# Kernel optimization log

Hardware: AMD Instinct MI355X
Metric: run time of the kernel (lower is better)

Reference implementation:

```python
import jax, jax.numpy as jnp
import numpy as np

B, N, XS, YS, KS, D, V = 32, 32, 256, 256, 128, 1024, 32000
TAU = 1e-4

def setup_inputs() -> dict:
    key = jax.random.key(0)
    ks = jax.random.split(key, 12)
    return {
        'utterence_hidden': jax.random.normal(ks[0], (XS, B, D), jnp.float32),
        'response_hidden': jax.random.normal(ks[1], (YS, B, D), jnp.float32),
        'knowledge_hidden': jax.random.normal(ks[2], (N, KS, B, D), jnp.float32),
        'utterence_pad_mask': jax.random.bernoulli(ks[3], 0.1, (B, XS)),
        'response_pad_mask': jax.random.bernoulli(ks[4], 0.1, (B, YS)),
        'knowledge_pad_mask': jax.random.bernoulli(ks[5], 0.1, (B, N, KS)),
        'gumbel': jax.random.gumbel(ks[6], (B, N), jnp.float32),
        'W1': jax.random.normal(ks[7], (D, 2 * D), jnp.float32) * 0.02,
        'b1': jnp.zeros((D,), jnp.float32),
        'W2': jax.random.normal(ks[8], (V, D), jnp.float32) * 0.02,
        'b2': jnp.zeros((V,), jnp.float32),
    }

def reference(utterence_hidden, response_hidden, knowledge_hidden,
              utterence_pad_mask, response_pad_mask, knowledge_pad_mask,
              gumbel, W1, b1, W2, b2):
    # make_pad_embed_zero's eye-matrix bmm/einsum is mathematically just masking
    uh = jnp.transpose(utterence_hidden, (1, 0, 2)) * (~utterence_pad_mask)[:, :, None]   # (B,XS,D)
    rh = jnp.transpose(response_hidden, (1, 0, 2)) * (~response_pad_mask)[:, :, None]     # (B,YS,D)
    kh = jnp.transpose(knowledge_hidden, (2, 0, 1, 3)) * (~knowledge_pad_mask)[..., None] # (B,N,KS,D)
    # AvgPool2d over full seq length == sum / seq_len (zeros included)
    mean_X = jnp.sum(uh, axis=1) / XS          # (B,D)
    mean_Y = jnp.sum(rh, axis=1) / YS          # (B,D)
    mean_K = jnp.sum(kh, axis=2) / KS          # (B,N,D)
    prior = jax.nn.log_softmax(jnp.einsum('bd,bnd->bn', mean_X, mean_K), axis=1)  # (B,N)
    X_cat_Y = jnp.concatenate([mean_X, mean_Y], axis=1) @ W1.T + b1               # (B,D)
    posterior_logits = jnp.einsum('bd,bnd->bn', X_cat_Y, mean_K)                  # (B,N)
    posterior = jax.nn.softmax(posterior_logits, axis=1)
    # gumbel_softmax with tau=1e-4 (soft, near one-hot)
    K_index = jax.nn.softmax((posterior_logits + gumbel) / TAU, axis=1)           # (B,N)
    selected_K = jnp.einsum('bnsd,bn->bsd', kh, K_index)                          # (B,KS,D)
    vocab_selected_K = jnp.einsum('bnd,bn->bd', mean_K, K_index)                  # (B,D)
    vocab_selected_K = jax.nn.log_softmax(vocab_selected_K @ W2.T + b2, axis=1)   # (B,V)
    return (prior, posterior, K_index, selected_K, vocab_selected_K)
```

## Files before the change

### kernel.cpp

```cpp
#include <hip/hip_runtime.h>
#include <math.h>

#define BB 32
#define NN 32
#define XSS 256
#define KSS 128
#define DD 1024
#define VV 32000
#define TAU_INV 10000.0f

typedef int mask_t;

#define WS_MEANX   0
#define WS_MEANY   32768
#define WS_MEANK   65536
#define WS_XCATY   1114112
#define WS_VPRE    1146880
#define WS_NNZ_CNT 1179648
#define WS_NNZ_IDX 1179680
#define WS_NNZ_W   1180704
#define WS_LSM_M   1181728
#define WS_LSM_S   1182240
#define WS_LSE     1182752

#define OUT_PRIOR  0
#define OUT_POST   (BB*NN)
#define OUT_KIDX   (2*BB*NN)
#define OUT_SEL    (3*BB*NN)
#define OUT_VOCAB  (3*BB*NN + BB*KSS*DD)

__device__ __forceinline__ float dot4(float4 a, float4 b) {
  return a.x*b.x + a.y*b.y + a.z*b.z + a.w*b.w;
}

__global__ void k_meanxy(const float4* __restrict__ U, const float4* __restrict__ R,
                         const mask_t* __restrict__ um, const mask_t* __restrict__ rm,
                         float* __restrict__ ws) {
  const int chunk = blockIdx.x, b = blockIdx.y, which = blockIdx.z, t = threadIdx.x;
  const float4* src = which ? R : U;
  const mask_t* m = which ? rm : um;
  float* dst = ws + (which ? WS_MEANY : WS_MEANX) + b * DD;
  float4 acc = make_float4(0.f, 0.f, 0.f, 0.f);
  const int x0 = chunk * 32;
  for (int x = x0; x < x0 + 32; ++x) {
    if (!m[b * XSS + x]) {
      float4 v = src[(x * BB + b) * (DD/4) + t];
      acc.x += v.x; acc.y += v.y; acc.z += v.z; acc.w += v.w;
    }
  }
  const float s = 1.0f / XSS;
  atomicAdd(&dst[t*4+0], acc.x * s);
  atomicAdd(&dst[t*4+1], acc.y * s);
  atomicAdd(&dst[t*4+2], acc.z * s);
  atomicAdd(&dst[t*4+3], acc.w * s);
}

__global__ void k_meank(const float4* __restrict__ K, const mask_t* __restrict__ km,
                        float* __restrict__ ws) {
  const int n = blockIdx.x, b = blockIdx.y, t = threadIdx.x;
  const mask_t* mrow = km + (b * NN + n) * KSS;
  float4 acc = make_float4(0.f, 0.f, 0.f, 0.f);
  #pragma unroll 2
  for (int s = 0; s < KSS; ++s) {
    if (!mrow[s]) {
      float4 v = K[((n * KSS + s) * BB + b) * (DD/4) + t];
      acc.x += v.x; acc.y += v.y; acc.z += v.z; acc.w += v.w;
    }
  }
  const float sc = 1.0f / KSS;
  float4* out = (float4*)(ws + WS_MEANK) + (b * NN + n) * (DD/4);
  out[t] = make_float4(acc.x*sc, acc.y*sc, acc.z*sc, acc.w*sc);
}

__global__ void k_xcaty(const float4* __restrict__ W1, const float* __restrict__ b1,
                        float* __restrict__ ws) {
  const int t = threadIdx.x;
  const int b = t & 31;
  const int d = blockIdx.x * 8 + (t >> 5);
  const float4* mx = (const float4*)(ws + WS_MEANX) + b * (DD/4);
  const float4* my = (const float4*)(ws + WS_MEANY) + b * (DD/4);
  const float4* w  = W1 + d * (2 * DD / 4);
  float acc = b1[d];
  #pragma unroll 4
  for (int q = 0; q < DD/4; ++q) acc += dot4(w[q], mx[q]);
  #pragma unroll 4
  for (int q = 0; q < DD/4; ++q) acc += dot4(w[DD/4 + q], my[q]);
  ws[WS_XCATY + b * DD + d] = acc;
}

__global__ void k_small(const float* __restrict__ gumbel, float* __restrict__ ws,
                        float* __restrict__ out) {
  const int b = blockIdx.x, t = threadIdx.x;
  const int lane = t & 63, wid = t >> 6;
  __shared__ float redp[4], redq[4];
  __shared__ float plp[NN], plq[NN], kw[NN];
  __shared__ float scal[3];
  __shared__ int   nnz_idx_s[NN];
  __shared__ float nnz_w_s[NN];
  __shared__ int   nnz_cnt_s;

  const float4* mk = (const float4*)(ws + WS_MEANK) + b * NN * (DD/4);
  const float4 mxr = ((const float4*)(ws + WS_MEANX))[b * (DD/4) + t];
  const float4 xyr = ((const float4*)(ws + WS_XCATY))[b * (DD/4) + t];

  for (int n = 0; n < NN; ++n) {
    float4 mkv = mk[n * (DD/4) + t];
    float pp = dot4(mkv, mxr);
    float qq = dot4(mkv, xyr);
    for (int off = 32; off > 0; off >>= 1) {
      pp += __shfl_down(pp, off);
      qq += __shfl_down(qq, off);
    }
    if (lane == 0) { redp[wid] = pp; redq[wid] = qq; }
    __syncthreads();
    if (t == 0) {
      plp[n] = redp[0] + redp[1] + redp[2] + redp[3];
      plq[n] = redq[0] + redq[1] + redq[2] + redq[3];
    }
    __syncthreads();
  }

  if (t == 0) {
    float z[NN];
    float m1 = -1e30f, m2 = -1e30f, m3 = -1e30f;
    for (int n = 0; n < NN; ++n) {
      m1 = fmaxf(m1, plp[n]);
      m2 = fmaxf(m2, plq[n]);
      z[n] = plq[n] + gumbel[b * NN + n];
      m3 = fmaxf(m3, z[n]);
    }
    float s1 = 0.f, s2 = 0.f, s3 = 0.f;
    for (int n = 0; n < NN; ++n) {
      s1 += expf(plp[n] - m1);
      s2 += expf(plq[n] - m2);
      float w = expf((z[n] - m3) * TAU_INV);
      kw[n] = w;
      s3 += w;
    }
    scal[0] = m1 + logf(s1);
    scal[1] = m2;
    scal[2] = s2;
    const float inv3 = 1.0f / s3;
    int cnt = 0;
    for (int n = 0; n < NN; ++n) {
      kw[n] *= inv3;
      if (kw[n] > 0.f) { nnz_idx_s[cnt] = n; nnz_w_s[cnt] = kw[n]; ++cnt; }
    }
    nnz_cnt_s = cnt;
    ((int*)(ws + WS_NNZ_CNT))[b] = cnt;
    for (int j = 0; j < cnt; ++j) {
      ((int*)(ws + WS_NNZ_IDX))[b * NN + j] = nnz_idx_s[j];
      ws[WS_NNZ_W + b * NN + j] = nnz_w_s[j];
    }
  }
  __syncthreads();

  if (t < NN) {
    out[OUT_PRIOR + b * NN + t] = plp[t] - scal[0];
    out[OUT_POST  + b * NN + t] = expf(plq[t] - scal[1]) / scal[2];
    out[OUT_KIDX  + b * NN + t] = kw[t];
  }

  float4 acc = make_float4(0.f, 0.f, 0.f, 0.f);
  const int cnt = nnz_cnt_s;
  for (int j = 0; j < cnt; ++j) {
    const float w = nnz_w_s[j];
    float4 v = mk[nnz_idx_s[j] * (DD/4) + t];
    acc.x += w * v.x; acc.y += w * v.y; acc.z += w * v.z; acc.w += w * v.w;
  }
  ((float4*)(ws + WS_VPRE))[b * (DD/4) + t] = acc;
}

__global__ void k_selected(const float4* __restrict__ K, const mask_t* __restrict__ km,
                           const float* __restrict__ ws, float4* __restrict__ outsel) {
  const int s = blockIdx.x, b = blockIdx.y, t = threadIdx.x;
  const int cnt = ((const int*)(ws + WS_NNZ_CNT))[b];
  float4 acc = make_float4(0.f, 0.f, 0.f, 0.f);
  for (int j = 0; j < cnt; ++j) {
    const int n = ((const int*)(ws + WS_NNZ_IDX))[b * NN + j];
    const float w = ws[WS_NNZ_W + b * NN + j];
    if (!km[(b * NN + n) * KSS + s]) {
      float4 v = K[((n * KSS + s) * BB + b) * (DD/4) + t];
      acc.x += w * v.x; acc.y += w * v.y; acc.z += w * v.z; acc.w += w * v.w;
    }
  }
  outsel[(b * KSS + s) * (DD/4) + t] = acc;
}

__global__ void __launch_bounds__(256) k_vocab(const float4* __restrict__ W2,
                                               const float* __restrict__ ws,
                                               float* __restrict__ logits) {
  const int t = threadIdx.x;
  const int V0 = blockIdx.x * 256;
  const int e4_base = blockIdx.y * 128;
  __shared__ float4 w2s[256 * 9];
  __shared__ float4 pres[32 * 9];
  const float4* vp = (const float4*)(ws + WS_VPRE);
  const int vlane = t & 31, bgrp = t >> 5;

  float acc[8][4];
  #pragma unroll
  for (int k = 0; k < 8; ++k)
    #pragma unroll
    for (int j = 0; j < 4; ++j) acc[k][j] = 0.f;

  for (int e4 = e4_base; e4 < e4_base + 128; e4 += 8) {
    #pragma unroll
    for (int k = 0; k < 8; ++k) {
      const int f = t + 256 * k;
      const int vr = f >> 3, q = f & 7;
      w2s[vr * 9 + q] = W2[(V0 + vr) * (DD/4) + e4 + q];
    }
    {
      const int br = t >> 3, q = t & 7;
      pres[br * 9 + q] = vp[br * (DD/4) + e4 + q];
    }
    __syncthreads();
    #pragma unroll
    for (int q = 0; q < 8; ++q) {
      float4 pb[4];
      #pragma unroll
      for (int j = 0; j < 4; ++j) pb[j] = pres[(bgrp + 8 * j) * 9 + q];
      #pragma unroll
      for (int k = 0; k < 8; ++k) {
        float4 wv = w2s[(vlane + 32 * k) * 9 + q];
        #pragma unroll
        for (int j = 0; j < 4; ++j) acc[k][j] += dot4(wv, pb[j]);
      }
    }
    __syncthreads();
  }
  #pragma unroll
  for (int k = 0; k < 8; ++k)
    #pragma unroll
    for (int j = 0; j < 4; ++j)
      atomicAdd(&logits[(bgrp + 8 * j) * VV + V0 + vlane + 32 * k], acc[k][j]);
}

__global__ void k_lsm1(const float* __restrict__ logits, const float* __restrict__ b2,
                       float* __restrict__ ws) {
  const int c = blockIdx.x, b = blockIdx.y, t = threadIdx.x;
  const int lane = t & 63, wid = t >> 6;
  const float* base = logits + b * VV + c * 2000;
  const float* bb = b2 + c * 2000;
  __shared__ float red[4];
  float xv[8];
  int cnt = 0;
  float m = -1e30f;
  for (int i = t; i < 2000; i += 256) {
    float x = base[i] + bb[i];
    xv[cnt++] = x;
    m = fmaxf(m, x);
  }
  for (int off = 32; off > 0; off >>= 1) m = fmaxf(m, __shfl_down(m, off));
  if (lane == 0) red[wid] = m;
  __syncthreads();
  if (t == 0) red[0] = fmaxf(fmaxf(red[0], red[1]), fmaxf(red[2], red[3]));
  __syncthreads();
  const float M = red[0];
  __syncthreads();
  float s = 0.f;
  for (int i = 0; i < cnt; ++i) s += expf(xv[i] - M);
  for (int off = 32; off > 0; off >>= 1) s += __shfl_down(s, off);
  if (lane == 0) red[wid] = s;
  __syncthreads();
  if (t == 0) {
    ws[WS_LSM_M + b * 16 + c] = M;
    ws[WS_LSM_S + b * 16 + c] = red[0] + red[1] + red[2] + red[3];
  }
}

__global__ void k_lsm2(float* __restrict__ ws) {
  const int t = threadIdx.x;
  if (t < BB) {
    float M = -1e30f;
    for (int c = 0; c < 16; ++c) M = fmaxf(M, ws[WS_LSM_M + t * 16 + c]);
    float S = 0.f;
    for (int c = 0; c < 16; ++c)
      S += ws[WS_LSM_S + t * 16 + c] * expf(ws[WS_LSM_M + t * 16 + c] - M);
    ws[WS_LSE + t] = M + logf(S);
  }
}

__global__ void k_lsm3(const float* __restrict__ b2, const float* __restrict__ ws,
                       float* __restrict__ logits) {
  const int v = blockIdx.x * 256 + threadIdx.x;
  const int b = blockIdx.y;
  logits[b * VV + v] = logits[b * VV + v] + b2[v] - ws[WS_LSE + b];
}

extern "C" void kernel_launch(void* const* d_in, const int* in_sizes, int n_in,
                              void* d_out, int out_size, void* d_ws, size_t ws_size,
                              hipStream_t stream) {
  const float4* U  = (const float4*)d_in[0];
  const float4* R  = (const float4*)d_in[1];
  const float4* K  = (const float4*)d_in[2];
  const mask_t* um = (const mask_t*)d_in[3];
  const mask_t* rm = (const mask_t*)d_in[4];
  const mask_t* km = (const mask_t*)d_in[5];
  const float* g   = (const float*)d_in[6];
  const float4* W1 = (const float4*)d_in[7];
  const float* b1  = (const float*)d_in[8];
  const float4* W2 = (const float4*)d_in[9];
  const float* b2  = (const float*)d_in[10];
  float* out = (float*)d_out;
  float* ws  = (float*)d_ws;

  hipMemsetAsync(ws + WS_MEANX, 0, 2 * BB * DD * sizeof(float), stream);
  hipMemsetAsync(out + OUT_VOCAB, 0, (size_t)BB * VV * sizeof(float), stream);

  k_meanxy <<<dim3(8, 32, 2), 256, 0, stream>>>(U, R, um, rm, ws);
  k_meank  <<<dim3(NN, BB),   256, 0, stream>>>(K, km, ws);
  k_xcaty  <<<dim3(128),      256, 0, stream>>>(W1, b1, ws);
  k_small  <<<dim3(BB),       256, 0, stream>>>(g, ws, out);
  k_selected<<<dim3(KSS, BB), 256, 0, stream>>>(K, km, ws, (float4*)(out + OUT_SEL));
  k_vocab  <<<dim3(125, 2),   256, 0, stream>>>(W2, ws, out + OUT_VOCAB);
  k_lsm1   <<<dim3(16, BB),   256, 0, stream>>>(out + OUT_VOCAB, b2, ws);
  k_lsm2   <<<dim3(1),        64,  0, stream>>>(ws);
  k_lsm3   <<<dim3(125, BB),  256, 0, stream>>>(b2, ws, out + OUT_VOCAB);
}
```

Measured before the change: 986.4 us.

## Rework mean, xcaty, small and vocab kernels; drop atomics and a launch

Several kernels change at once. k_meanxy uses a branchless mask-weighted loop over larger chunks. k_meank compacts unmasked rows with a ballot so that four loads are in flight at a time. k_xcaty tiles W1 and the inputs through shared memory so each weight is reused across batches. k_small reduces per wave with no per-n barriers, and k_vocab writes two partial buffers instead of doing atomicAdd, which removes the memset and the k_lsm2 launch. This adds workspace traffic for the partial logits, but the work is mostly bound by the memory read of K.

```diff
diff --git a/kernel.cpp b/kernel.cpp
--- a/kernel.cpp
+++ b/kernel.cpp
@@ -21,7 +21,8 @@
 #define WS_NNZ_W   1180704
 #define WS_LSM_M   1181728
 #define WS_LSM_S   1182240
-#define WS_LSE     1182752
+#define WS_VP0     1183744
+#define WS_VP1     2207744
 
 #define OUT_PRIOR  0
 #define OUT_POST   (BB*NN)
@@ -31,6 +32,9 @@
 
 __device__ __forceinline__ float dot4(float4 a, float4 b) {
   return a.x*b.x + a.y*b.y + a.z*b.z + a.w*b.w;
+}
+__device__ __forceinline__ void fma4(float4& a, float w, float4 v) {
+  a.x += w*v.x; a.y += w*v.y; a.z += w*v.z; a.w += w*v.w;
 }
 
 __global__ void k_meanxy(const float4* __restrict__ U, const float4* __restrict__ R,
@@ -40,13 +44,15 @@
   const float4* src = which ? R : U;
   const mask_t* m = which ? rm : um;
   float* dst = ws + (which ? WS_MEANY : WS_MEANX) + b * DD;
+  __shared__ float wmask[64];
+  const int x0 = chunk * 64;
+  if (t < 64) wmask[t] = m[b * XSS + x0 + t] ? 0.f : 1.f;
+  __syncthreads();
   float4 acc = make_float4(0.f, 0.f, 0.f, 0.f);
-  const int x0 = chunk * 32;
-  for (int x = x0; x < x0 + 32; ++x) {
-    if (!m[b * XSS + x]) {
-      float4 v = src[(x * BB + b) * (DD/4) + t];
-      acc.x += v.x; acc.y += v.y; acc.z += v.z; acc.w += v.w;
-    }
+  #pragma unroll 4
+  for (int i = 0; i < 64; ++i) {
+    float4 v = src[((x0 + i) * BB + b) * (DD/4) + t];
+    fma4(acc, wmask[i], v);
   }
   const float s = 1.0f / XSS;
   atomicAdd(&dst[t*4+0], acc.x * s);
@@ -58,41 +64,90 @@
 __global__ void k_meank(const float4* __restrict__ K, const mask_t* __restrict__ km,
                         float* __restrict__ ws) {
   const int n = blockIdx.x, b = blockIdx.y, t = threadIdx.x;
+  const int lane = t & 63, wid = t >> 6;
+  __shared__ int idx[KSS];
+  __shared__ int wcnt[2];
   const mask_t* mrow = km + (b * NN + n) * KSS;
-  float4 acc = make_float4(0.f, 0.f, 0.f, 0.f);
-  #pragma unroll 2
-  for (int s = 0; s < KSS; ++s) {
-    if (!mrow[s]) {
-      float4 v = K[((n * KSS + s) * BB + b) * (DD/4) + t];
-      acc.x += v.x; acc.y += v.y; acc.z += v.z; acc.w += v.w;
-    }
+  bool keep = false; int pre = 0;
+  if (t < KSS) {
+    keep = !mrow[t];
+    unsigned long long mb = __ballot(keep);
+    pre = __popcll(mb & ((1ull << lane) - 1ull));
+    if (lane == 0) wcnt[wid] = __popcll(mb);
+  }
+  __syncthreads();
+  if (t < KSS && keep) {
+    const int base = wid ? wcnt[0] : 0;
+    idx[base + pre] = t;
+  }
+  __syncthreads();
+  const int cnt = wcnt[0] + wcnt[1];
+  const float4* Kb = K + (size_t)b * (DD/4);
+  const size_t srow = (size_t)BB * (DD/4);
+  float4 a = make_float4(0.f, 0.f, 0.f, 0.f);
+  int j = 0;
+  for (; j + 4 <= cnt; j += 4) {
+    const int s0 = idx[j], s1 = idx[j+1], s2 = idx[j+2], s3 = idx[j+3];
+    float4 v0 = Kb[(size_t)(n*KSS + s0) * srow + t];
+    float4 v1 = Kb[(size_t)(n*KSS + s1) * srow + t];
+    float4 v2 = Kb[(size_t)(n*KSS + s2) * srow + t];
+    float4 v3 = Kb[(size_t)(n*KSS + s3) * srow + t];
+    a.x += (v0.x + v1.x) + (v2.x + v3.x);
+    a.y += (v0.y + v1.y) + (v2.y + v3.y);
+    a.z += (v0.z + v1.z) + (v2.z + v3.z);
+    a.w += (v0.w + v1.w) + (v2.w + v3.w);
+  }
+  for (; j < cnt; ++j) {
+    float4 v = Kb[(size_t)(n*KSS + idx[j]) * srow + t];
+    a.x += v.x; a.y += v.y; a.z += v.z; a.w += v.w;
   }
   const float sc = 1.0f / KSS;
-  float4* out = (float4*)(ws + WS_MEANK) + (b * NN + n) * (DD/4);
-  out[t] = make_float4(acc.x*sc, acc.y*sc, acc.z*sc, acc.w*sc);
+  ((float4*)(ws + WS_MEANK))[(b * NN + n) * (DD/4) + t] =
+      make_float4(a.x*sc, a.y*sc, a.z*sc, a.w*sc);
 }
 
 __global__ void k_xcaty(const float4* __restrict__ W1, const float* __restrict__ b1,
                         float* __restrict__ ws) {
+  __shared__ float4 xys[32][33];
+  __shared__ float4 w1s[16][33];
   const int t = threadIdx.x;
-  const int b = t & 31;
-  const int d = blockIdx.x * 8 + (t >> 5);
-  const float4* mx = (const float4*)(ws + WS_MEANX) + b * (DD/4);
-  const float4* my = (const float4*)(ws + WS_MEANY) + b * (DD/4);
-  const float4* w  = W1 + d * (2 * DD / 4);
-  float acc = b1[d];
-  #pragma unroll 4
-  for (int q = 0; q < DD/4; ++q) acc += dot4(w[q], mx[q]);
-  #pragma unroll 4
-  for (int q = 0; q < DD/4; ++q) acc += dot4(w[DD/4 + q], my[q]);
-  ws[WS_XCATY + b * DD + d] = acc;
+  const int d0 = blockIdx.x * 16;
+  const int dl = t >> 4, bg = t & 15;
+  const float4* mx = (const float4*)(ws + WS_MEANX);
+  const float4* my = (const float4*)(ws + WS_MEANY);
+  float acc[2] = {0.f, 0.f};
+  for (int c = 0; c < 16; ++c) {
+    #pragma unroll
+    for (int i = 0; i < 4; ++i) {
+      const int f = t + 256 * i;
+      const int br = f >> 5, q = f & 31;
+      const int kf4 = c * 32 + q;
+      xys[br][q] = (kf4 < 256) ? mx[br * 256 + kf4] : my[br * 256 + (kf4 - 256)];
+    }
+    #pragma unroll
+    for (int i = 0; i < 2; ++i) {
+      const int f = t + 256 * i;
+      const int dr = f >> 5, q = f & 31;
+      w1s[dr][q] = W1[(d0 + dr) * (2*DD/4) + c * 32 + q];
+    }
+    __syncthreads();
+    #pragma unroll
+    for (int q = 0; q < 32; ++q) {
+      const float4 wv = w1s[dl][q];
+      acc[0] += dot4(wv, xys[bg*2+0][q]);
+      acc[1] += dot4(wv, xys[bg*2+1][q]);
+    }
+    __syncthreads();
+  }
+  const float bias = b1[d0 + dl];
+  ws[WS_XCATY + (bg*2+0) * DD + d0 + dl] = acc[0] + bias;
+  ws[WS_XCATY + (bg*2+1) * DD + d0 + dl] = acc[1] + bias;
 }
 
 __global__ void k_small(const float* __restrict__ gumbel, float* __restrict__ ws,
                         float* __restrict__ out) {
   const int b = blockIdx.x, t = threadIdx.x;
   const int lane = t & 63, wid = t >> 6;
-  __shared__ float redp[4], redq[4];
   __shared__ float plp[NN], plq[NN], kw[NN];
   __shared__ float scal[3];
   __shared__ int   nnz_idx_s[NN];
@@ -100,25 +155,25 @@
   __shared__ int   nnz_cnt_s;
 
   const float4* mk = (const float4*)(ws + WS_MEANK) + b * NN * (DD/4);
-  const float4 mxr = ((const float4*)(ws + WS_MEANX))[b * (DD/4) + t];
-  const float4 xyr = ((const float4*)(ws + WS_XCATY))[b * (DD/4) + t];
-
-  for (int n = 0; n < NN; ++n) {
-    float4 mkv = mk[n * (DD/4) + t];
-    float pp = dot4(mkv, mxr);
-    float qq = dot4(mkv, xyr);
+  const float4* mx = (const float4*)(ws + WS_MEANX) + b * (DD/4);
+  const float4* xy = (const float4*)(ws + WS_XCATY) + b * (DD/4);
+
+  for (int n = wid; n < NN; n += 4) {
+    float pp = 0.f, qq = 0.f;
+    #pragma unroll
+    for (int r = 0; r < 4; ++r) {
+      const int q = r * 64 + lane;
+      const float4 mkv = mk[n * (DD/4) + q];
+      pp += dot4(mkv, mx[q]);
+      qq += dot4(mkv, xy[q]);
+    }
     for (int off = 32; off > 0; off >>= 1) {
       pp += __shfl_down(pp, off);
       qq += __shfl_down(qq, off);
     }
-    if (lane == 0) { redp[wid] = pp; redq[wid] = qq; }
-    __syncthreads();
-    if (t == 0) {
-      plp[n] = redp[0] + redp[1] + redp[2] + redp[3];
-      plq[n] = redq[0] + redq[1] + redq[2] + redq[3];
-    }
-    __syncthreads();
-  }
+    if (lane == 0) { plp[n] = pp; plq[n] = qq; }
+  }
+  __syncthreads();
 
   if (t == 0) {
     float z[NN];
@@ -165,8 +220,7 @@
   const int cnt = nnz_cnt_s;
   for (int j = 0; j < cnt; ++j) {
     const float w = nnz_w_s[j];
-    float4 v = mk[nnz_idx_s[j] * (DD/4) + t];
-    acc.x += w * v.x; acc.y += w * v.y; acc.z += w * v.z; acc.w += w * v.w;
+    fma4(acc, w, mk[nnz_idx_s[j] * (DD/4) + t]);
   }
   ((float4*)(ws + WS_VPRE))[b * (DD/4) + t] = acc;
 }
@@ -180,19 +234,18 @@
     const int n = ((const int*)(ws + WS_NNZ_IDX))[b * NN + j];
     const float w = ws[WS_NNZ_W + b * NN + j];
     if (!km[(b * NN + n) * KSS + s]) {
-      float4 v = K[((n * KSS + s) * BB + b) * (DD/4) + t];
-      acc.x += w * v.x; acc.y += w * v.y; acc.z += w * v.z; acc.w += w * v.w;
+      fma4(acc, w, K[((n * KSS + s) * BB + b) * (DD/4) + t]);
     }
   }
   outsel[(b * KSS + s) * (DD/4) + t] = acc;
 }
 
 __global__ void __launch_bounds__(256) k_vocab(const float4* __restrict__ W2,
-                                               const float* __restrict__ ws,
-                                               float* __restrict__ logits) {
+                                               float* __restrict__ ws) {
   const int t = threadIdx.x;
   const int V0 = blockIdx.x * 256;
   const int e4_base = blockIdx.y * 128;
+  float* part = ws + (blockIdx.y ? WS_VP1 : WS_VP0);
   __shared__ float4 w2s[256 * 9];
   __shared__ float4 pres[32 * 9];
   const float4* vp = (const float4*)(ws + WS_VPRE);
@@ -234,21 +287,21 @@
   for (int k = 0; k < 8; ++k)
     #pragma unroll
     for (int j = 0; j < 4; ++j)
-      atomicAdd(&logits[(bgrp + 8 * j) * VV + V0 + vlane + 32 * k], acc[k][j]);
-}
-
-__global__ void k_lsm1(const float* __restrict__ logits, const float* __restrict__ b2,
-                       float* __restrict__ ws) {
+      part[(bgrp + 8 * j) * VV + V0 + vlane + 32 * k] = acc[k][j];
+}
+
+__global__ void k_lsm1(const float* __restrict__ b2, float* __restrict__ ws) {
   const int c = blockIdx.x, b = blockIdx.y, t = threadIdx.x;
   const int lane = t & 63, wid = t >> 6;
-  const float* base = logits + b * VV + c * 2000;
+  const float* p0 = ws + WS_VP0 + b * VV + c * 2000;
+  const float* p1 = ws + WS_VP1 + b * VV + c * 2000;
   const float* bb = b2 + c * 2000;
   __shared__ float red[4];
   float xv[8];
   int cnt = 0;
   float m = -1e30f;
   for (int i = t; i < 2000; i += 256) {
-    float x = base[i] + bb[i];
+    float x = p0[i] + p1[i] + bb[i];
     xv[cnt++] = x;
     m = fmaxf(m, x);
   }
@@ -270,23 +323,22 @@
   }
 }
 
-__global__ void k_lsm2(float* __restrict__ ws) {
-  const int t = threadIdx.x;
-  if (t < BB) {
+__global__ void k_lsm3(const float* __restrict__ b2, const float* __restrict__ ws,
+                       float* __restrict__ logits) {
+  const int b = blockIdx.y, t = threadIdx.x;
+  __shared__ float lse_s;
+  if (t == 0) {
     float M = -1e30f;
-    for (int c = 0; c < 16; ++c) M = fmaxf(M, ws[WS_LSM_M + t * 16 + c]);
+    for (int c = 0; c < 16; ++c) M = fmaxf(M, ws[WS_LSM_M + b * 16 + c]);
     float S = 0.f;
     for (int c = 0; c < 16; ++c)
-      S += ws[WS_LSM_S + t * 16 + c] * expf(ws[WS_LSM_M + t * 16 + c] - M);
-    ws[WS_LSE + t] = M + logf(S);
-  }
-}
-
-__global__ void k_lsm3(const float* __restrict__ b2, const float* __restrict__ ws,
-                       float* __restrict__ logits) {
-  const int v = blockIdx.x * 256 + threadIdx.x;
-  const int b = blockIdx.y;
-  logits[b * VV + v] = logits[b * VV + v] + b2[v] - ws[WS_LSE + b];
+      S += ws[WS_LSM_S + b * 16 + c] * expf(ws[WS_LSM_M + b * 16 + c] - M);
+    lse_s = M + logf(S);
+  }
+  __syncthreads();
+  const int v = blockIdx.x * 256 + t;
+  logits[b * VV + v] = ws[WS_VP0 + b * VV + v] + ws[WS_VP1 + b * VV + v]
+                       + b2[v] - lse_s;
 }
 
 extern "C" void kernel_launch(void* const* d_in, const int* in_sizes, int n_in,
@@ -307,15 +359,13 @@
   float* ws  = (float*)d_ws;
 
   hipMemsetAsync(ws + WS_MEANX, 0, 2 * BB * DD * sizeof(float), stream);
-  hipMemsetAsync(out + OUT_VOCAB, 0, (size_t)BB * VV * sizeof(float), stream);
-
-  k_meanxy <<<dim3(8, 32, 2), 256, 0, stream>>>(U, R, um, rm, ws);
-  k_meank  <<<dim3(NN, BB),   256, 0, stream>>>(K, km, ws);
-  k_xcaty  <<<dim3(128),      256, 0, stream>>>(W1, b1, ws);
-  k_small  <<<dim3(BB),       256, 0, stream>>>(g, ws, out);
-  k_selected<<<dim3(KSS, BB), 256, 0, stream>>>(K, km, ws, (float4*)(out + OUT_SEL));
-  k_vocab  <<<dim3(125, 2),   256, 0, stream>>>(W2, ws, out + OUT_VOCAB);
-  k_lsm1   <<<dim3(16, BB),   256, 0, stream>>>(out + OUT_VOCAB, b2, ws);
-  k_lsm2   <<<dim3(1),        64,  0, stream>>>(ws);
-  k_lsm3   <<<dim3(125, BB),  256, 0, stream>>>(b2, ws, out + OUT_VOCAB);
-}
+
+  k_meanxy  <<<dim3(4, 32, 2), 256, 0, stream>>>(U, R, um, rm, ws);
+  k_meank   <<<dim3(NN, BB),   256, 0, stream>>>(K, km, ws);
+  k_xcaty   <<<dim3(64),       256, 0, stream>>>(W1, b1, ws);
+  k_small   <<<dim3(BB),       256, 0, stream>>>(g, ws, out);
+  k_selected<<<dim3(KSS, BB),  256, 0, stream>>>(K, km, ws, (float4*)(out + OUT_SEL));
+  k_vocab   <<<dim3(125, 2),   256, 0, stream>>>(W2, ws);
+  k_lsm1    <<<dim3(16, BB),   256, 0, stream>>>(b2, ws);
+  k_lsm3    <<<dim3(125, BB),  256, 0, stream>>>(b2, ws, out + OUT_VOCAB);
+}
```

New measurement: 941.8 us. 4.5% less time.
